# Optimization experiments

Hardware: AMD Instinct MI355X
Metric: run time of the kernel (lower is better)

The kernel has to match this reference:

```python
import jax, jax.numpy as jnp
import numpy as np

N, E = 50000, 800000
DIM, H, D = 256, 16, 8          # dim, num_heads, qk_dim
DH = D * H                      # 128
IN_RPE = 18
SCALE = D ** -0.5               # default qk_scale (None -> 1/sqrt(qk_dim))
EPS = 1e-16                     # torch_geometric softmax denominator eps


def setup_inputs() -> dict:
    key = jax.random.key(0)
    ks = jax.random.split(key, 10)
    x = jax.random.normal(ks[0], (N, DIM), dtype=jnp.float32)
    edge_index = jax.random.randint(ks[1], (2, E), 0, N, dtype=jnp.int64)
    edge_attr = jax.random.normal(ks[2], (E, IN_RPE), dtype=jnp.float32)
    # qkv Linear(dim -> 2*D*H + dim)
    Wqkv = jax.random.normal(ks[3], (DIM, 2 * DH + DIM), dtype=jnp.float32) * DIM ** -0.5
    bqkv = jnp.zeros((2 * DH + DIM,), dtype=jnp.float32)
    # k_rpe / q_rpe Linear(in_rpe_dim -> D*H) (heads_share_rpe=False)
    Wk_rpe = jax.random.normal(ks[4], (IN_RPE, DH), dtype=jnp.float32) * IN_RPE ** -0.5
    bk_rpe = jnp.zeros((DH,), dtype=jnp.float32)
    Wq_rpe = jax.random.normal(ks[5], (IN_RPE, DH), dtype=jnp.float32) * IN_RPE ** -0.5
    bq_rpe = jnp.zeros((DH,), dtype=jnp.float32)
    return {"x": x, "edge_index": edge_index, "edge_attr": edge_attr,
            "Wqkv": Wqkv, "bqkv": bqkv,
            "Wk_rpe": Wk_rpe, "bk_rpe": bk_rpe,
            "Wq_rpe": Wq_rpe, "bq_rpe": bq_rpe}


def _segment_softmax(compat, s, num_nodes):
    # numerically-stable softmax over edges grouped by source node s; compat: (E,H)
    m = jax.ops.segment_max(compat, s, num_segments=num_nodes)   # (N,H)
    ex = jnp.exp(compat - m[s])
    den = jax.ops.segment_sum(ex, s, num_segments=num_nodes)     # (N,H)
    return ex / (den[s] + EPS)


def reference(x, edge_index, edge_attr, Wqkv, bqkv, Wk_rpe, bk_rpe, Wq_rpe, bq_rpe):
    n = x.shape[0]
    e = edge_index.shape[1]
    qkv = x @ Wqkv + bqkv                      # (N, 2*DH + DIM)
    q = qkv[:, :DH].reshape(n, H, D)
    k = qkv[:, DH:2 * DH].reshape(n, H, D)
    v = qkv[:, 2 * DH:].reshape(n, H, DIM // H)
    s, t = edge_index[0], edge_index[1]
    qe = q[s] * SCALE                          # (E,H,D)
    ke = k[t]
    ke = ke + (edge_attr @ Wk_rpe + bk_rpe).reshape(e, H, D)
    qe = qe + (edge_attr @ Wq_rpe + bq_rpe).reshape(e, H, D)
    compat = jnp.einsum('ehd,ehd->eh', qe, ke)  # (E,H)
    attn = _segment_softmax(compat, s, n)       # (E,H)
    msg = (v[t] * attn[..., None]).reshape(e, DIM)  # (E,DIM)
    out = jax.ops.segment_sum(msg, s, num_segments=n)  # (N,DIM)
    return out
```

## Files before the change

### kernel.cpp

```cpp
#include <hip/hip_runtime.h>
#include <math.h>

#define DIMX   256
#define HEADS  16
#define QKD    8
#define DH     128
#define QKVW   512
#define INRPE  18
#define SCALE  0.35355339059327373f

typedef __attribute__((ext_vector_type(8))) short bf16x8;
typedef __attribute__((ext_vector_type(4))) float f32x4;

__device__ __forceinline__ void split1(float v, unsigned short& h, unsigned short& l)
{
    unsigned b  = __float_as_uint(v);
    unsigned hb = (b + 0x7FFFu + ((b >> 16) & 1u)) & 0xFFFF0000u;
    h = (unsigned short)(hb >> 16);
    float r = v - __uint_as_float(hb);
    unsigned rb = __float_as_uint(r);
    l = (unsigned short)((rb + 0x7FFFu + ((rb >> 16) & 1u)) >> 16);
}

__global__ __launch_bounds__(256) void convert_x(
    const float* __restrict__ x, unsigned short* __restrict__ xh,
    unsigned short* __restrict__ xl, int Nn, int Mpad)
{
    size_t total = (size_t)Mpad * 64;
    for (size_t i = (size_t)blockIdx.x * blockDim.x + threadIdx.x; i < total;
         i += (size_t)gridDim.x * blockDim.x) {
        size_t row = i >> 6;
        float4 v = make_float4(0.f, 0.f, 0.f, 0.f);
        if (row < (size_t)Nn) v = *(const float4*)&x[i * 4];
        ushort4 h, l;
        split1(v.x, h.x, l.x);
        split1(v.y, h.y, l.y);
        split1(v.z, h.z, l.z);
        split1(v.w, h.w, l.w);
        *(ushort4*)&xh[i * 4] = h;
        *(ushort4*)&xl[i * 4] = l;
    }
}

__global__ __launch_bounds__(256) void convert_w(
    const float* __restrict__ W, unsigned short* __restrict__ wth,
    unsigned short* __restrict__ wtl)
{
    int n = blockIdx.x;
    int k = threadIdx.x;
    float v = W[(size_t)k * QKVW + n];
    unsigned short h, l;
    split1(v, h, l);
    wth[(size_t)n * DIMX + k] = h;
    wtl[(size_t)n * DIMX + k] = l;
}

__global__ __launch_bounds__(256, 2) void qkv_gemm_mfma(
    const unsigned short* __restrict__ xh, const unsigned short* __restrict__ xl,
    const unsigned short* __restrict__ wth, const unsigned short* __restrict__ wtl,
    const float* __restrict__ bias, float* __restrict__ qkv, int Nn)
{
    int tid  = threadIdx.x;
    int w    = tid >> 6, lane = tid & 63;
    int wm   = w >> 1,   wn   = w & 1;
    int row0 = blockIdx.x * 128 + wm * 64;
    int col0 = blockIdx.y * 128 + wn * 64;
    int lrow = lane & 15;
    int lk8  = (lane >> 4) * 8;

    const unsigned short* pah = xh  + (size_t)(row0 + lrow) * DIMX + lk8;
    const unsigned short* pal = xl  + (size_t)(row0 + lrow) * DIMX + lk8;
    const unsigned short* pbh = wth + (size_t)(col0 + lrow) * DIMX + lk8;
    const unsigned short* pbl = wtl + (size_t)(col0 + lrow) * DIMX + lk8;

    f32x4 acc[4][4];
    #pragma unroll
    for (int i = 0; i < 4; i++)
        #pragma unroll
        for (int j = 0; j < 4; j++)
            acc[i][j] = (f32x4){0.f, 0.f, 0.f, 0.f};

    for (int t = 0; t < DIMX / 32; ++t) {
        int kb = t * 32;
        bf16x8 ah[4], al[4], bh[4], bl[4];
        #pragma unroll
        for (int f = 0; f < 4; ++f) {
            ah[f] = *(const bf16x8*)(pah + (size_t)f * 4096 + kb);
            al[f] = *(const bf16x8*)(pal + (size_t)f * 4096 + kb);
            bh[f] = *(const bf16x8*)(pbh + (size_t)f * 4096 + kb);
            bl[f] = *(const bf16x8*)(pbl + (size_t)f * 4096 + kb);
        }
        #pragma unroll
        for (int fm = 0; fm < 4; ++fm)
            #pragma unroll
            for (int fn = 0; fn < 4; ++fn) {
                acc[fm][fn] = __builtin_amdgcn_mfma_f32_16x16x32_bf16(
                    ah[fm], bh[fn], acc[fm][fn], 0, 0, 0);
                acc[fm][fn] = __builtin_amdgcn_mfma_f32_16x16x32_bf16(
                    ah[fm], bl[fn], acc[fm][fn], 0, 0, 0);
                acc[fm][fn] = __builtin_amdgcn_mfma_f32_16x16x32_bf16(
                    al[fm], bh[fn], acc[fm][fn], 0, 0, 0);
            }
    }

    float sc = (blockIdx.y == 0) ? SCALE : 1.0f;
    int rbase = (lane >> 4) * 4;
    #pragma unroll
    for (int fn = 0; fn < 4; ++fn) {
        float bv = bias[col0 + fn * 16 + lrow];
        #pragma unroll
        for (int fm = 0; fm < 4; ++fm) {
            #pragma unroll
            for (int j = 0; j < 4; ++j) {
                int r = row0 + fm * 16 + rbase + j;
                if (r < Nn)
                    qkv[(size_t)r * QKVW + col0 + fn * 16 + lrow] =
                        (acc[fm][fn][j] + bv) * sc;
            }
        }
    }
}

__global__ __launch_bounds__(256) void qkv_gemm(
    const float* __restrict__ x, const float* __restrict__ W,
    const float* __restrict__ bias, float* __restrict__ qkv, int Nn)
{
    __shared__ float As[16][132];
    __shared__ float Bs[16][132];

    int tid  = threadIdx.x;
    int row0 = blockIdx.x * 128;
    int col0 = blockIdx.y * 128;
    int tx = tid & 15, ty = tid >> 4;

    float acc[8][8] = {};

    for (int k0 = 0; k0 < DIMX; k0 += 16) {
        #pragma unroll
        for (int r = 0; r < 2; r++) {
            int idx  = tid + r * 256;
            int arow = idx >> 2, acol = (idx & 3) * 4;
            float4 av = make_float4(0.f, 0.f, 0.f, 0.f);
            int grow = row0 + arow;
            if (grow < Nn) av = *(const float4*)&x[(size_t)grow * DIMX + k0 + acol];
            As[acol + 0][arow] = av.x;
            As[acol + 1][arow] = av.y;
            As[acol + 2][arow] = av.z;
            As[acol + 3][arow] = av.w;
        }
        #pragma unroll
        for (int r = 0; r < 2; r++) {
            int idx  = tid + r * 256;
            int brow = idx >> 5, bcol = (idx & 31) * 4;
            float4 bv = *(const float4*)&W[(size_t)(k0 + brow) * QKVW + col0 + bcol];
            *(float4*)&Bs[brow][bcol] = bv;
        }
        __syncthreads();
        #pragma unroll
        for (int kk = 0; kk < 16; kk++) {
            float a0[8], b0[8];
            *(float4*)&a0[0] = *(const float4*)&As[kk][ty * 8];
            *(float4*)&a0[4] = *(const float4*)&As[kk][ty * 8 + 4];
            *(float4*)&b0[0] = *(const float4*)&Bs[kk][tx * 4];
            *(float4*)&b0[4] = *(const float4*)&Bs[kk][64 + tx * 4];
            #pragma unroll
            for (int i = 0; i < 8; i++)
                #pragma unroll
                for (int j = 0; j < 8; j++)
                    acc[i][j] = fmaf(a0[i], b0[j], acc[i][j]);
        }
        __syncthreads();
    }

    float4 bv0 = *(const float4*)&bias[col0 + tx * 4];
    float4 bv1 = *(const float4*)&bias[col0 + 64 + tx * 4];
    float sc = (col0 == 0) ? SCALE : 1.0f;
    #pragma unroll
    for (int i = 0; i < 8; i++) {
        int grow = row0 + ty * 8 + i;
        if (grow < Nn) {
            float4 o0, o1;
            o0.x = (acc[i][0] + bv0.x) * sc;
            o0.y = (acc[i][1] + bv0.y) * sc;
            o0.z = (acc[i][2] + bv0.z) * sc;
            o0.w = (acc[i][3] + bv0.w) * sc;
            o1.x = (acc[i][4] + bv1.x) * sc;
            o1.y = (acc[i][5] + bv1.y) * sc;
            o1.z = (acc[i][6] + bv1.z) * sc;
            o1.w = (acc[i][7] + bv1.w) * sc;
            *(float4*)&qkv[(size_t)grow * QKVW + col0 + tx * 4] = o0;
            *(float4*)&qkv[(size_t)grow * QKVW + col0 + 64 + tx * 4] = o1;
        }
    }
}

__global__ void count_kernel(const int* __restrict__ ei, int* __restrict__ deg, int E)
{
    int e = blockIdx.x * blockDim.x + threadIdx.x;
    if (e < E) atomicAdd(&deg[ei[e]], 1);
}

__device__ __forceinline__ int4 load_deg4(const int* __restrict__ deg, int base, int n)
{
    int4 v = make_int4(0, 0, 0, 0);
    if (base + 3 < n) v = *(const int4*)&deg[base];
    else {
        if (base + 0 < n) v.x = deg[base + 0];
        if (base + 1 < n) v.y = deg[base + 1];
        if (base + 2 < n) v.z = deg[base + 2];
        if (base + 3 < n) v.w = deg[base + 3];
    }
    return v;
}

__global__ __launch_bounds__(256) void scan_sums(
    const int* __restrict__ deg, int* __restrict__ psum, int n)
{
    int base = blockIdx.x * 1024 + threadIdx.x * 4;
    int4 v = load_deg4(deg, base, n);
    int s = v.x + v.y + v.z + v.w;
    #pragma unroll
    for (int d = 1; d < 64; d <<= 1) s += __shfl_xor(s, d, 64);
    __shared__ int ws[4];
    int lane = threadIdx.x & 63, w = threadIdx.x >> 6;
    if (lane == 0) ws[w] = s;
    __syncthreads();
    if (threadIdx.x == 0) psum[blockIdx.x] = ws[0] + ws[1] + ws[2] + ws[3];
}

__global__ __launch_bounds__(64) void scan_base(
    const int* __restrict__ psum, int* __restrict__ pbase,
    int* __restrict__ off, int n, int nchunk)
{
    int t = threadIdx.x;
    int carry = 0;
    for (int base = 0; base < nchunk; base += 64) {
        int v = (base + t < nchunk) ? psum[base + t] : 0;
        int incl = v;
        #pragma unroll
        for (int d = 1; d < 64; d <<= 1) {
            int u = __shfl_up(incl, d, 64);
            if (t >= d) incl += u;
        }
        if (base + t < nchunk) pbase[base + t] = carry + incl - v;
        carry += __shfl(incl, 63, 64);
    }
    if (t == 0) off[n] = carry;
}

__global__ __launch_bounds__(256) void scan_final(
    const int* __restrict__ deg, const int* __restrict__ pbase,
    int* __restrict__ off, int n)
{
    int base = blockIdx.x * 1024 + threadIdx.x * 4;
    int4 v = load_deg4(deg, base, n);
    int e1 = v.x, e2 = e1 + v.y, e3 = e2 + v.z, T = e3 + v.w;
    int lane = threadIdx.x & 63, w = threadIdx.x >> 6;
    int incl = T;
    #pragma unroll
    for (int d = 1; d < 64; d <<= 1) {
        int u = __shfl_up(incl, d, 64);
        if (lane >= d) incl += u;
    }
    int lexcl = incl - T;
    __shared__ int ws[4];
    if (lane == 63) ws[w] = incl;
    __syncthreads();
    int wexcl = 0;
    #pragma unroll
    for (int j = 0; j < 4; j++) if (j < w) wexcl += ws[j];
    int o0 = pbase[blockIdx.x] + wexcl + lexcl;
    if (base + 0 < n) off[base + 0] = o0;
    if (base + 1 < n) off[base + 1] = o0 + e1;
    if (base + 2 < n) off[base + 2] = o0 + e2;
    if (base + 3 < n) off[base + 3] = o0 + e3;
}

__global__ void scatter_kernel(const int* __restrict__ ei,
                               const int* __restrict__ off, int* __restrict__ cur,
                               int2* __restrict__ elist, int E)
{
    int e = blockIdx.x * blockDim.x + threadIdx.x;
    if (e < E) {
        int s = ei[e];
        int t = ei[E + e];
        int pos = atomicAdd(&cur[s], 1);
        elist[off[s] + pos] = make_int2(e, t);
    }
}

__global__ __launch_bounds__(128, 2) void node_attn(
    const float* __restrict__ qkv, const int2* __restrict__ elist,
    const int* __restrict__ off, const float* __restrict__ edge_attr,
    const float* __restrict__ Wq_rpe, const float* __restrict__ bq_rpe,
    const float* __restrict__ Wk_rpe, const float* __restrict__ bk_rpe,
    float* __restrict__ out, int Nn)
{
    int tid = threadIdx.x;

    float wq[INRPE], wk[INRPE];
    #pragma unroll
    for (int j = 0; j < INRPE; j++) {
        wq[j] = Wq_rpe[j * DH + tid];
        wk[j] = Wk_rpe[j * DH + tid];
    }
    #pragma unroll
    for (int j = 0; j < INRPE; j++) {
        asm volatile("" : "+v"(wq[j]), "+v"(wk[j]));
    }
    float bqv = bq_rpe[tid];
    float bkv = bk_rpe[tid];

    for (int n = blockIdx.x; n < Nn; n += gridDim.x) {
        int beg = off[n], end = off[n + 1];
        if (beg == end) {
            *(float2*)&out[(size_t)n * DIMX + 2 * tid] = make_float2(0.f, 0.f);
            continue;
        }
        float qs = qkv[(size_t)n * QKVW + tid] + bqv;

        float lsum = 0.0f;
        float2 o = make_float2(0.f, 0.f);

        int2 etA = elist[beg];
        int eA = __builtin_amdgcn_readfirstlane(etA.x);
        float  ktA = qkv[(size_t)etA.y * QKVW + DH + tid];
        float2 vtA = *(const float2*)&qkv[(size_t)etA.y * QKVW + 2 * DH + 2 * tid];
        float eaA[INRPE];
        {
            const float2* p = (const float2*)(edge_attr + (size_t)eA * INRPE);
            #pragma unroll
            for (int j = 0; j < 9; j++) { float2 u = p[j]; eaA[2*j] = u.x; eaA[2*j+1] = u.y; }
        }

        for (int i = beg; i < end; i += 2) {
            bool hasB = (i + 1 < end);
            float ktB = 0.f; float2 vtB = make_float2(0.f, 0.f);
            float eaB[INRPE];
            if (hasB) {
                int2 etB = elist[i + 1];
                int eB = __builtin_amdgcn_readfirstlane(etB.x);
                ktB = qkv[(size_t)etB.y * QKVW + DH + tid];
                vtB = *(const float2*)&qkv[(size_t)etB.y * QKVW + 2 * DH + 2 * tid];
                const float2* p = (const float2*)(edge_attr + (size_t)eB * INRPE);
                #pragma unroll
                for (int j = 0; j < 9; j++) { float2 u = p[j]; eaB[2*j] = u.x; eaB[2*j+1] = u.y; }
            }

            {
                float qr = 0.f, kr = bkv;
                #pragma unroll
                for (int j = 0; j < INRPE; j++) {
                    qr = fmaf(eaA[j], wq[j], qr);
                    kr = fmaf(eaA[j], wk[j], kr);
                }
                float c2 = (qs + qr) * (ktA + kr);
                c2 += __shfl_xor(c2, 1, 64);
                c2 += __shfl_xor(c2, 2, 64);
                c2 += __shfl_xor(c2, 4, 64);
                float ex = __expf(c2);
                lsum += ex;
                o.x = fmaf(ex, vtA.x, o.x);
                o.y = fmaf(ex, vtA.y, o.y);
            }

            if (i + 2 < end) {
                int2 et2 = elist[i + 2];
                int eN = __builtin_amdgcn_readfirstlane(et2.x);
                ktA = qkv[(size_t)et2.y * QKVW + DH + tid];
                vtA = *(const float2*)&qkv[(size_t)et2.y * QKVW + 2 * DH + 2 * tid];
                const float2* p = (const float2*)(edge_attr + (size_t)eN * INRPE);
                #pragma unroll
                for (int j = 0; j < 9; j++) { float2 u = p[j]; eaA[2*j] = u.x; eaA[2*j+1] = u.y; }
            }

            if (hasB) {
                float qr = 0.f, kr = bkv;
                #pragma unroll
                for (int j = 0; j < INRPE; j++) {
                    qr = fmaf(eaB[j], wq[j], qr);
                    kr = fmaf(eaB[j], wk[j], kr);
                }
                float c2 = (qs + qr) * (ktB + kr);
                c2 += __shfl_xor(c2, 1, 64);
                c2 += __shfl_xor(c2, 2, 64);
                c2 += __shfl_xor(c2, 4, 64);
                float ex = __expf(c2);
                lsum += ex;
                o.x = fmaf(ex, vtB.x, o.x);
                o.y = fmaf(ex, vtB.y, o.y);
            }
        }

        float inv = 1.0f / (lsum + 1e-16f);
        *(float2*)&out[(size_t)n * DIMX + 2 * tid] = make_float2(o.x * inv, o.y * inv);
    }
}

extern "C" void kernel_launch(void* const* d_in, const int* in_sizes, int n_in,
                              void* d_out, int out_size, void* d_ws, size_t ws_size,
                              hipStream_t stream)
{
    const float* x    = (const float*)d_in[0];
    const int*   ei   = (const int*)d_in[1];
    const float* ea   = (const float*)d_in[2];
    const float* Wqkv = (const float*)d_in[3];
    const float* bqkv = (const float*)d_in[4];
    const float* Wk   = (const float*)d_in[5];
    const float* bk   = (const float*)d_in[6];
    const float* Wq   = (const float*)d_in[7];
    const float* bq   = (const float*)d_in[8];

    int Nn = in_sizes[0] / DIMX;
    int E  = in_sizes[1] / 2;
    float* out = (float*)d_out;

    int Mblocks = (Nn + 127) / 128;
    int Mpad    = Mblocks * 128;
    int nchunk  = (Nn + 1023) / 1024;

    size_t qkv_bytes  = (size_t)Nn * QKVW * sizeof(float);
    float* qkv = (float*)d_ws;
    char*  P   = (char*)d_ws + qkv_bytes;

    size_t xpart  = (size_t)Mpad * DIMX * sizeof(unsigned short);
    size_t wpart  = (size_t)QKVW * DIMX * sizeof(unsigned short);
    size_t gemm_bytes = 2 * xpart + 2 * wpart;
    size_t csr_bytes  = sizeof(int) * (size_t)(3 * Nn + 2 + 2 * nchunk + 8)
                      + sizeof(int2) * (size_t)E;
    size_t need = qkv_bytes + (gemm_bytes > csr_bytes ? gemm_bytes : csr_bytes);

    int*  deg = (int*)P;
    int*  cur = deg + Nn;
    int*  off = cur + Nn;
    int2* elist = (int2*)(off + ((Nn + 2) & ~1));
    int*  psum  = (int*)(elist + E);
    int*  pbase = psum + nchunk;

    if (ws_size >= need) {
        unsigned short* xh  = (unsigned short*)P;
        unsigned short* xl  = xh + (size_t)Mpad * DIMX;
        unsigned short* wth = xl + (size_t)Mpad * DIMX;
        unsigned short* wtl = wth + (size_t)QKVW * DIMX;

        convert_x<<<2048, 256, 0, stream>>>(x, xh, xl, Nn, Mpad);
        convert_w<<<QKVW, 256, 0, stream>>>(Wqkv, wth, wtl);
        qkv_gemm_mfma<<<dim3(Mblocks, 4), 256, 0, stream>>>(xh, xl, wth, wtl,
                                                            bqkv, qkv, Nn);
    } else {
        qkv_gemm<<<dim3(Mblocks, QKVW / 128), 256, 0, stream>>>(x, Wqkv, bqkv, qkv, Nn);
    }

    hipMemsetAsync(deg, 0, sizeof(int) * 2 * (size_t)Nn, stream);
    count_kernel<<<(E + 255) / 256, 256, 0, stream>>>(ei, deg, E);
    scan_sums<<<nchunk, 256, 0, stream>>>(deg, psum, Nn);
    scan_base<<<1, 64, 0, stream>>>(psum, pbase, off, Nn, nchunk);
    scan_final<<<nchunk, 256, 0, stream>>>(deg, pbase, off, Nn);
    scatter_kernel<<<(E + 255) / 256, 256, 0, stream>>>(ei, off, cur, elist, E);

    int nb = 4096 < Nn ? 4096 : Nn;
    node_attn<<<nb, 128, 0, stream>>>(qkv, elist, off, ea, Wq, bq, Wk, bk, out, Nn);
}
```

Before: 656.3 us.

## Store V in bf16, split QK/V buffers, one block per node with prefetch

Measured after the change: 569.4 us. 13.2% less time.

```diff
diff --git a/kernel.cpp b/kernel.cpp
--- a/kernel.cpp
+++ b/kernel.cpp
@@ -20,6 +20,17 @@
     float r = v - __uint_as_float(hb);
     unsigned rb = __float_as_uint(r);
     l = (unsigned short)((rb + 0x7FFFu + ((rb >> 16) & 1u)) >> 16);
+}
+
+__device__ __forceinline__ unsigned short f2bf(float v)
+{
+    unsigned b = __float_as_uint(v);
+    return (unsigned short)((b + 0x7FFFu + ((b >> 16) & 1u)) >> 16);
+}
+
+__device__ __forceinline__ float bf2f(unsigned short u)
+{
+    return __uint_as_float((unsigned)u << 16);
 }
 
 __global__ __launch_bounds__(256) void convert_x(
@@ -58,7 +69,8 @@
 __global__ __launch_bounds__(256, 2) void qkv_gemm_mfma(
     const unsigned short* __restrict__ xh, const unsigned short* __restrict__ xl,
     const unsigned short* __restrict__ wth, const unsigned short* __restrict__ wtl,
-    const float* __restrict__ bias, float* __restrict__ qkv, int Nn)
+    const float* __restrict__ bias, float* __restrict__ qk,
+    unsigned short* __restrict__ vb, int Nn)
 {
     int tid  = threadIdx.x;
     int w    = tid >> 6, lane = tid & 63;
@@ -103,27 +115,44 @@
             }
     }
 
-    float sc = (blockIdx.y == 0) ? SCALE : 1.0f;
     int rbase = (lane >> 4) * 4;
-    #pragma unroll
-    for (int fn = 0; fn < 4; ++fn) {
-        float bv = bias[col0 + fn * 16 + lrow];
-        #pragma unroll
-        for (int fm = 0; fm < 4; ++fm) {
+    if (blockIdx.y < 2) {
+        float sc = (blockIdx.y == 0) ? SCALE : 1.0f;
+        #pragma unroll
+        for (int fn = 0; fn < 4; ++fn) {
+            float bv = bias[col0 + fn * 16 + lrow];
             #pragma unroll
-            for (int j = 0; j < 4; ++j) {
-                int r = row0 + fm * 16 + rbase + j;
-                if (r < Nn)
-                    qkv[(size_t)r * QKVW + col0 + fn * 16 + lrow] =
-                        (acc[fm][fn][j] + bv) * sc;
-            }
+            for (int fm = 0; fm < 4; ++fm)
+                #pragma unroll
+                for (int j = 0; j < 4; ++j) {
+                    int r = row0 + fm * 16 + rbase + j;
+                    if (r < Nn)
+                        qk[(size_t)r * 256 + col0 + fn * 16 + lrow] =
+                            (acc[fm][fn][j] + bv) * sc;
+                }
+        }
+    } else {
+        int vcol0 = col0 - 256;
+        #pragma unroll
+        for (int fn = 0; fn < 4; ++fn) {
+            float bv = bias[col0 + fn * 16 + lrow];
+            #pragma unroll
+            for (int fm = 0; fm < 4; ++fm)
+                #pragma unroll
+                for (int j = 0; j < 4; ++j) {
+                    int r = row0 + fm * 16 + rbase + j;
+                    if (r < Nn)
+                        vb[(size_t)r * 256 + vcol0 + fn * 16 + lrow] =
+                            f2bf(acc[fm][fn][j] + bv);
+                }
         }
     }
 }
 
 __global__ __launch_bounds__(256) void qkv_gemm(
     const float* __restrict__ x, const float* __restrict__ W,
-    const float* __restrict__ bias, float* __restrict__ qkv, int Nn)
+    const float* __restrict__ bias, float* __restrict__ qk,
+    unsigned short* __restrict__ vb, int Nn)
 {
     __shared__ float As[16][132];
     __shared__ float Bs[16][132];
@@ -174,22 +203,31 @@
 
     float4 bv0 = *(const float4*)&bias[col0 + tx * 4];
     float4 bv1 = *(const float4*)&bias[col0 + 64 + tx * 4];
+    bool isv = (col0 >= 256);
     float sc = (col0 == 0) ? SCALE : 1.0f;
     #pragma unroll
     for (int i = 0; i < 8; i++) {
         int grow = row0 + ty * 8 + i;
         if (grow < Nn) {
-            float4 o0, o1;
-            o0.x = (acc[i][0] + bv0.x) * sc;
-            o0.y = (acc[i][1] + bv0.y) * sc;
-            o0.z = (acc[i][2] + bv0.z) * sc;
-            o0.w = (acc[i][3] + bv0.w) * sc;
-            o1.x = (acc[i][4] + bv1.x) * sc;
-            o1.y = (acc[i][5] + bv1.y) * sc;
-            o1.z = (acc[i][6] + bv1.z) * sc;
-            o1.w = (acc[i][7] + bv1.w) * sc;
-            *(float4*)&qkv[(size_t)grow * QKVW + col0 + tx * 4] = o0;
-            *(float4*)&qkv[(size_t)grow * QKVW + col0 + 64 + tx * 4] = o1;
+            float o0[4], o1[4];
+            o0[0] = (acc[i][0] + bv0.x) * sc;
+            o0[1] = (acc[i][1] + bv0.y) * sc;
+            o0[2] = (acc[i][2] + bv0.z) * sc;
+            o0[3] = (acc[i][3] + bv0.w) * sc;
+            o1[0] = (acc[i][4] + bv1.x) * sc;
+            o1[1] = (acc[i][5] + bv1.y) * sc;
+            o1[2] = (acc[i][6] + bv1.z) * sc;
+            o1[3] = (acc[i][7] + bv1.w) * sc;
+            if (!isv) {
+                *(float4*)&qk[(size_t)grow * 256 + col0 + tx * 4] = *(float4*)o0;
+                *(float4*)&qk[(size_t)grow * 256 + col0 + 64 + tx * 4] = *(float4*)o1;
+            } else {
+                int vc = col0 - 256;
+                ushort4 u0 = make_ushort4(f2bf(o0[0]), f2bf(o0[1]), f2bf(o0[2]), f2bf(o0[3]));
+                ushort4 u1 = make_ushort4(f2bf(o1[0]), f2bf(o1[1]), f2bf(o1[2]), f2bf(o1[3]));
+                *(ushort4*)&vb[(size_t)grow * 256 + vc + tx * 4] = u0;
+                *(ushort4*)&vb[(size_t)grow * 256 + vc + 64 + tx * 4] = u1;
+            }
         }
     }
 }
@@ -290,13 +328,16 @@
 }
 
 __global__ __launch_bounds__(128, 2) void node_attn(
-    const float* __restrict__ qkv, const int2* __restrict__ elist,
-    const int* __restrict__ off, const float* __restrict__ edge_attr,
+    const float* __restrict__ qk, const unsigned short* __restrict__ vb,
+    const int2* __restrict__ elist, const int* __restrict__ off,
+    const float* __restrict__ edge_attr,
     const float* __restrict__ Wq_rpe, const float* __restrict__ bq_rpe,
     const float* __restrict__ Wk_rpe, const float* __restrict__ bk_rpe,
     float* __restrict__ out, int Nn)
 {
     int tid = threadIdx.x;
+    int n = blockIdx.x;
+    if (n >= Nn) return;
 
     float wq[INRPE], wk[INRPE];
     #pragma unroll
@@ -308,93 +349,69 @@
     for (int j = 0; j < INRPE; j++) {
         asm volatile("" : "+v"(wq[j]), "+v"(wk[j]));
     }
-    float bqv = bq_rpe[tid];
-    float bkv = bk_rpe[tid];
-
-    for (int n = blockIdx.x; n < Nn; n += gridDim.x) {
-        int beg = off[n], end = off[n + 1];
-        if (beg == end) {
-            *(float2*)&out[(size_t)n * DIMX + 2 * tid] = make_float2(0.f, 0.f);
-            continue;
-        }
-        float qs = qkv[(size_t)n * QKVW + tid] + bqv;
-
-        float lsum = 0.0f;
-        float2 o = make_float2(0.f, 0.f);
-
-        int2 etA = elist[beg];
-        int eA = __builtin_amdgcn_readfirstlane(etA.x);
-        float  ktA = qkv[(size_t)etA.y * QKVW + DH + tid];
-        float2 vtA = *(const float2*)&qkv[(size_t)etA.y * QKVW + 2 * DH + 2 * tid];
-        float eaA[INRPE];
+
+    float qs = qk[(size_t)n * 256 + tid] + bq_rpe[tid];
+    float bk = bk_rpe[tid];
+
+    int beg = off[n], end = off[n + 1];
+
+    if (beg == end) {
+        *(float2*)&out[(size_t)n * DIMX + 2 * tid] = make_float2(0.f, 0.f);
+        return;
+    }
+
+    float lsum = 0.0f;
+    float2 o = make_float2(0.f, 0.f);
+
+    int2 etc = elist[beg];
+    float   ktc = qk[(size_t)etc.y * 256 + DH + tid];
+    ushort2 vtc = *(const ushort2*)&vb[(size_t)etc.y * 256 + 2 * tid];
+    float eac[INRPE];
+    {
+        const float2* p = (const float2*)(edge_attr + (size_t)etc.x * INRPE);
+        #pragma unroll
+        for (int j = 0; j < 9; j++) { float2 v2 = p[j]; eac[2*j] = v2.x; eac[2*j+1] = v2.y; }
+    }
+    int2 etn = elist[(beg + 1 < end) ? beg + 1 : beg];
+
+    #pragma unroll 1
+    for (int i = beg; i < end; i++) {
+        int inx2 = (i + 2 < end) ? i + 2 : end - 1;
+        int2 et2 = elist[inx2];
+        float   ktn = qk[(size_t)etn.y * 256 + DH + tid];
+        ushort2 vtn = *(const ushort2*)&vb[(size_t)etn.y * 256 + 2 * tid];
+        float ean[INRPE];
         {
-            const float2* p = (const float2*)(edge_attr + (size_t)eA * INRPE);
+            const float2* p = (const float2*)(edge_attr + (size_t)etn.x * INRPE);
             #pragma unroll
-            for (int j = 0; j < 9; j++) { float2 u = p[j]; eaA[2*j] = u.x; eaA[2*j+1] = u.y; }
-        }
-
-        for (int i = beg; i < end; i += 2) {
-            bool hasB = (i + 1 < end);
-            float ktB = 0.f; float2 vtB = make_float2(0.f, 0.f);
-            float eaB[INRPE];
-            if (hasB) {
-                int2 etB = elist[i + 1];
-                int eB = __builtin_amdgcn_readfirstlane(etB.x);
-                ktB = qkv[(size_t)etB.y * QKVW + DH + tid];
-                vtB = *(const float2*)&qkv[(size_t)etB.y * QKVW + 2 * DH + 2 * tid];
-                const float2* p = (const float2*)(edge_attr + (size_t)eB * INRPE);
-                #pragma unroll
-                for (int j = 0; j < 9; j++) { float2 u = p[j]; eaB[2*j] = u.x; eaB[2*j+1] = u.y; }
-            }
-
-            {
-                float qr = 0.f, kr = bkv;
-                #pragma unroll
-                for (int j = 0; j < INRPE; j++) {
-                    qr = fmaf(eaA[j], wq[j], qr);
-                    kr = fmaf(eaA[j], wk[j], kr);
-                }
-                float c2 = (qs + qr) * (ktA + kr);
-                c2 += __shfl_xor(c2, 1, 64);
-                c2 += __shfl_xor(c2, 2, 64);
-                c2 += __shfl_xor(c2, 4, 64);
-                float ex = __expf(c2);
-                lsum += ex;
-                o.x = fmaf(ex, vtA.x, o.x);
-                o.y = fmaf(ex, vtA.y, o.y);
-            }
-
-            if (i + 2 < end) {
-                int2 et2 = elist[i + 2];
-                int eN = __builtin_amdgcn_readfirstlane(et2.x);
-                ktA = qkv[(size_t)et2.y * QKVW + DH + tid];
-                vtA = *(const float2*)&qkv[(size_t)et2.y * QKVW + 2 * DH + 2 * tid];
-                const float2* p = (const float2*)(edge_attr + (size_t)eN * INRPE);
-                #pragma unroll
-                for (int j = 0; j < 9; j++) { float2 u = p[j]; eaA[2*j] = u.x; eaA[2*j+1] = u.y; }
-            }
-
-            if (hasB) {
-                float qr = 0.f, kr = bkv;
-                #pragma unroll
-                for (int j = 0; j < INRPE; j++) {
-                    qr = fmaf(eaB[j], wq[j], qr);
-                    kr = fmaf(eaB[j], wk[j], kr);
-                }
-                float c2 = (qs + qr) * (ktB + kr);
-                c2 += __shfl_xor(c2, 1, 64);
-                c2 += __shfl_xor(c2, 2, 64);
-                c2 += __shfl_xor(c2, 4, 64);
-                float ex = __expf(c2);
-                lsum += ex;
-                o.x = fmaf(ex, vtB.x, o.x);
-                o.y = fmaf(ex, vtB.y, o.y);
-            }
-        }
-
-        float inv = 1.0f / (lsum + 1e-16f);
-        *(float2*)&out[(size_t)n * DIMX + 2 * tid] = make_float2(o.x * inv, o.y * inv);
-    }
+            for (int j = 0; j < 9; j++) { float2 v2 = p[j]; ean[2*j] = v2.x; ean[2*j+1] = v2.y; }
+        }
+
+        float qr = 0.f, kr = bk;
+        #pragma unroll
+        for (int j = 0; j < INRPE; j++) {
+            qr = fmaf(eac[j], wq[j], qr);
+            kr = fmaf(eac[j], wk[j], kr);
+        }
+
+        float c2 = (qs + qr) * (ktc + kr);
+        c2 += __shfl_xor(c2, 1, 64);
+        c2 += __shfl_xor(c2, 2, 64);
+        c2 += __shfl_xor(c2, 4, 64);
+
+        float ex = __expf(c2);
+        lsum += ex;
+        o.x = fmaf(ex, bf2f(vtc.x), o.x);
+        o.y = fmaf(ex, bf2f(vtc.y), o.y);
+
+        etc = etn; etn = et2;
+        ktc = ktn; vtc = vtn;
+        #pragma unroll
+        for (int j = 0; j < INRPE; j++) eac[j] = ean[j];
+    }
+
+    float inv = 1.0f / (lsum + 1e-16f);
+    *(float2*)&out[(size_t)n * DIMX + 2 * tid] = make_float2(o.x * inv, o.y * inv);
 }
 
 extern "C" void kernel_launch(void* const* d_in, const int* in_sizes, int n_in,
@@ -419,16 +436,19 @@
     int Mpad    = Mblocks * 128;
     int nchunk  = (Nn + 1023) / 1024;
 
-    size_t qkv_bytes  = (size_t)Nn * QKVW * sizeof(float);
-    float* qkv = (float*)d_ws;
-    char*  P   = (char*)d_ws + qkv_bytes;
+    size_t qk_bytes = (size_t)Nn * 256 * sizeof(float);
+    size_t vb_bytes = (size_t)Nn * 256 * sizeof(unsigned short);
+    float*          qkbuf = (float*)d_ws;
+    unsigned short* vbbuf = (unsigned short*)((char*)d_ws + qk_bytes);
+    char*           P     = (char*)d_ws + qk_bytes + vb_bytes;
 
     size_t xpart  = (size_t)Mpad * DIMX * sizeof(unsigned short);
     size_t wpart  = (size_t)QKVW * DIMX * sizeof(unsigned short);
     size_t gemm_bytes = 2 * xpart + 2 * wpart;
     size_t csr_bytes  = sizeof(int) * (size_t)(3 * Nn + 2 + 2 * nchunk + 8)
                       + sizeof(int2) * (size_t)E;
-    size_t need = qkv_bytes + (gemm_bytes > csr_bytes ? gemm_bytes : csr_bytes);
+    size_t need = qk_bytes + vb_bytes
+                + (gemm_bytes > csr_bytes ? gemm_bytes : csr_bytes);
 
     int*  deg = (int*)P;
     int*  cur = deg + Nn;
@@ -446,9 +466,10 @@
         convert_x<<<2048, 256, 0, stream>>>(x, xh, xl, Nn, Mpad);
         convert_w<<<QKVW, 256, 0, stream>>>(Wqkv, wth, wtl);
         qkv_gemm_mfma<<<dim3(Mblocks, 4), 256, 0, stream>>>(xh, xl, wth, wtl,
-                                                            bqkv, qkv, Nn);
+                                                            bqkv, qkbuf, vbbuf, Nn);
     } else {
-        qkv_gemm<<<dim3(Mblocks, QKVW / 128), 256, 0, stream>>>(x, Wqkv, bqkv, qkv, Nn);
+        qkv_gemm<<<dim3(Mblocks, QKVW / 128), 256, 0, stream>>>(x, Wqkv, bqkv,
+                                                                qkbuf, vbbuf, Nn);
     }
 
     hipMemsetAsync(deg, 0, sizeof(int) * 2 * (size_t)Nn, stream);
@@ -458,6 +479,6 @@
     scan_final<<<nchunk, 256, 0, stream>>>(deg, pbase, off, Nn);
     scatter_kernel<<<(E + 255) / 256, 256, 0, stream>>>(ei, off, cur, elist, E);
 
-    int nb = 4096 < Nn ? 4096 : Nn;
-    node_attn<<<nb, 128, 0, stream>>>(qkv, elist, off, ea, Wq, bq, Wk, bk, out, Nn);
-}
+    node_attn<<<Nn, 128, 0, stream>>>(qkbuf, vbbuf, elist, off, ea,
+                                      Wq, bq, Wk, bk, out, Nn);
+}
```

## Store K/V in fp16 split buffer and launch one block per node

Applied to the files above, without the earlier changes.

Measured after the change: 787.9 us. 20.1% more time.

```diff
diff --git a/kernel.cpp b/kernel.cpp
--- a/kernel.cpp
+++ b/kernel.cpp
@@ -1,4 +1,5 @@
 #include <hip/hip_runtime.h>
+#include <hip/hip_fp16.h>
 #include <math.h>
 
 #define DIMX   256
@@ -6,6 +7,7 @@
 #define QKD    8
 #define DH     128
 #define QKVW   512
+#define KVW    384
 #define INRPE  18
 #define SCALE  0.35355339059327373f
 
@@ -55,10 +57,11 @@
     wtl[(size_t)n * DIMX + k] = l;
 }
 
-__global__ __launch_bounds__(256, 2) void qkv_gemm_mfma(
+__global__ __launch_bounds__(256, 3) void qkv_gemm_mfma(
     const unsigned short* __restrict__ xh, const unsigned short* __restrict__ xl,
     const unsigned short* __restrict__ wth, const unsigned short* __restrict__ wtl,
-    const float* __restrict__ bias, float* __restrict__ qkv, int Nn)
+    const float* __restrict__ bias, float* __restrict__ qbuf,
+    __half* __restrict__ kvb, int Nn)
 {
     int tid  = threadIdx.x;
     int w    = tid >> 6, lane = tid & 63;
@@ -103,27 +106,43 @@
             }
     }
 
-    float sc = (blockIdx.y == 0) ? SCALE : 1.0f;
     int rbase = (lane >> 4) * 4;
-    #pragma unroll
-    for (int fn = 0; fn < 4; ++fn) {
-        float bv = bias[col0 + fn * 16 + lrow];
-        #pragma unroll
-        for (int fm = 0; fm < 4; ++fm) {
-            #pragma unroll
-            for (int j = 0; j < 4; ++j) {
-                int r = row0 + fm * 16 + rbase + j;
-                if (r < Nn)
-                    qkv[(size_t)r * QKVW + col0 + fn * 16 + lrow] =
-                        (acc[fm][fn][j] + bv) * sc;
-            }
+    if (blockIdx.y == 0) {
+        #pragma unroll
+        for (int fn = 0; fn < 4; ++fn) {
+            float bv = bias[col0 + fn * 16 + lrow];
+            #pragma unroll
+            for (int fm = 0; fm < 4; ++fm)
+                #pragma unroll
+                for (int j = 0; j < 4; ++j) {
+                    int r = row0 + fm * 16 + rbase + j;
+                    if (r < Nn)
+                        qbuf[(size_t)r * DH + col0 + fn * 16 + lrow] =
+                            (acc[fm][fn][j] + bv) * SCALE;
+                }
+        }
+    } else {
+        int base = col0 - 128;
+        #pragma unroll
+        for (int fn = 0; fn < 4; ++fn) {
+            float bv = bias[col0 + fn * 16 + lrow];
+            #pragma unroll
+            for (int fm = 0; fm < 4; ++fm)
+                #pragma unroll
+                for (int j = 0; j < 4; ++j) {
+                    int r = row0 + fm * 16 + rbase + j;
+                    if (r < Nn)
+                        kvb[(size_t)r * KVW + base + fn * 16 + lrow] =
+                            __float2half(acc[fm][fn][j] + bv);
+                }
         }
     }
 }
 
 __global__ __launch_bounds__(256) void qkv_gemm(
     const float* __restrict__ x, const float* __restrict__ W,
-    const float* __restrict__ bias, float* __restrict__ qkv, int Nn)
+    const float* __restrict__ bias, float* __restrict__ qbuf,
+    __half* __restrict__ kvb, int Nn)
 {
     __shared__ float As[16][132];
     __shared__ float Bs[16][132];
@@ -174,22 +193,29 @@
 
     float4 bv0 = *(const float4*)&bias[col0 + tx * 4];
     float4 bv1 = *(const float4*)&bias[col0 + 64 + tx * 4];
-    float sc = (col0 == 0) ? SCALE : 1.0f;
     #pragma unroll
     for (int i = 0; i < 8; i++) {
         int grow = row0 + ty * 8 + i;
         if (grow < Nn) {
-            float4 o0, o1;
-            o0.x = (acc[i][0] + bv0.x) * sc;
-            o0.y = (acc[i][1] + bv0.y) * sc;
-            o0.z = (acc[i][2] + bv0.z) * sc;
-            o0.w = (acc[i][3] + bv0.w) * sc;
-            o1.x = (acc[i][4] + bv1.x) * sc;
-            o1.y = (acc[i][5] + bv1.y) * sc;
-            o1.z = (acc[i][6] + bv1.z) * sc;
-            o1.w = (acc[i][7] + bv1.w) * sc;
-            *(float4*)&qkv[(size_t)grow * QKVW + col0 + tx * 4] = o0;
-            *(float4*)&qkv[(size_t)grow * QKVW + col0 + 64 + tx * 4] = o1;
+            float o0[4], o1[4];
+            o0[0] = acc[i][0] + bv0.x; o0[1] = acc[i][1] + bv0.y;
+            o0[2] = acc[i][2] + bv0.z; o0[3] = acc[i][3] + bv0.w;
+            o1[0] = acc[i][4] + bv1.x; o1[1] = acc[i][5] + bv1.y;
+            o1[2] = acc[i][6] + bv1.z; o1[3] = acc[i][7] + bv1.w;
+            if (col0 == 0) {
+                #pragma unroll
+                for (int j = 0; j < 4; j++) {
+                    qbuf[(size_t)grow * DH + tx * 4 + j]      = o0[j] * SCALE;
+                    qbuf[(size_t)grow * DH + 64 + tx * 4 + j] = o1[j] * SCALE;
+                }
+            } else {
+                int base = col0 - 128;
+                #pragma unroll
+                for (int j = 0; j < 4; j++) {
+                    kvb[(size_t)grow * KVW + base + tx * 4 + j]      = __float2half(o0[j]);
+                    kvb[(size_t)grow * KVW + base + 64 + tx * 4 + j] = __float2half(o1[j]);
+                }
+            }
         }
     }
 }
@@ -290,13 +316,15 @@
 }
 
 __global__ __launch_bounds__(128, 2) void node_attn(
-    const float* __restrict__ qkv, const int2* __restrict__ elist,
-    const int* __restrict__ off, const float* __restrict__ edge_attr,
+    const float* __restrict__ qbuf, const __half* __restrict__ kv,
+    const int2* __restrict__ elist, const int* __restrict__ off,
+    const float* __restrict__ edge_attr,
     const float* __restrict__ Wq_rpe, const float* __restrict__ bq_rpe,
     const float* __restrict__ Wk_rpe, const float* __restrict__ bk_rpe,
     float* __restrict__ out, int Nn)
 {
     int tid = threadIdx.x;
+    int n = blockIdx.x;
 
     float wq[INRPE], wk[INRPE];
     #pragma unroll
@@ -308,93 +336,91 @@
     for (int j = 0; j < INRPE; j++) {
         asm volatile("" : "+v"(wq[j]), "+v"(wk[j]));
     }
-    float bqv = bq_rpe[tid];
+
+    float qs = qbuf[(size_t)n * DH + tid] + bq_rpe[tid];
     float bkv = bk_rpe[tid];
 
-    for (int n = blockIdx.x; n < Nn; n += gridDim.x) {
-        int beg = off[n], end = off[n + 1];
-        if (beg == end) {
-            *(float2*)&out[(size_t)n * DIMX + 2 * tid] = make_float2(0.f, 0.f);
-            continue;
-        }
-        float qs = qkv[(size_t)n * QKVW + tid] + bqv;
-
-        float lsum = 0.0f;
-        float2 o = make_float2(0.f, 0.f);
-
-        int2 etA = elist[beg];
-        int eA = __builtin_amdgcn_readfirstlane(etA.x);
-        float  ktA = qkv[(size_t)etA.y * QKVW + DH + tid];
-        float2 vtA = *(const float2*)&qkv[(size_t)etA.y * QKVW + 2 * DH + 2 * tid];
-        float eaA[INRPE];
+    int beg = off[n], end = off[n + 1];
+    if (beg == end) {
+        *(float2*)&out[(size_t)n * DIMX + 2 * tid] = make_float2(0.f, 0.f);
+        return;
+    }
+
+    float lsum = 0.0f;
+    float2 o = make_float2(0.f, 0.f);
+
+    int2 etA = elist[beg];
+    __half  kA = kv[(size_t)etA.y * KVW + tid];
+    __half2 vA = *(const __half2*)&kv[(size_t)etA.y * KVW + DH + 2 * tid];
+    float eaA[INRPE];
+    {
+        const float2* p = (const float2*)(edge_attr + (size_t)etA.x * INRPE);
+        #pragma unroll
+        for (int j = 0; j < 9; j++) { float2 u = p[j]; eaA[2*j] = u.x; eaA[2*j+1] = u.y; }
+    }
+
+    for (int i = beg; i < end; i += 2) {
+        bool hasB = (i + 1 < end);
+        __half kB = __float2half(0.f);
+        __half2 vB = __half2(__float2half(0.f), __float2half(0.f));
+        float eaB[INRPE];
+        if (hasB) {
+            int2 etB = elist[i + 1];
+            kB = kv[(size_t)etB.y * KVW + tid];
+            vB = *(const __half2*)&kv[(size_t)etB.y * KVW + DH + 2 * tid];
+            const float2* p = (const float2*)(edge_attr + (size_t)etB.x * INRPE);
+            #pragma unroll
+            for (int j = 0; j < 9; j++) { float2 u = p[j]; eaB[2*j] = u.x; eaB[2*j+1] = u.y; }
+        }
+
         {
-            const float2* p = (const float2*)(edge_attr + (size_t)eA * INRPE);
+            float qr = 0.f, kr = bkv;
+            #pragma unroll
+            for (int j = 0; j < INRPE; j++) {
+                qr = fmaf(eaA[j], wq[j], qr);
+                kr = fmaf(eaA[j], wk[j], kr);
+            }
+            float c2 = (qs + qr) * (__half2float(kA) + kr);
+            c2 += __shfl_xor(c2, 1, 64);
+            c2 += __shfl_xor(c2, 2, 64);
+            c2 += __shfl_xor(c2, 4, 64);
+            float ex = __expf(c2);
+            float2 vf = __half22float2(vA);
+            lsum += ex;
+            o.x = fmaf(ex, vf.x, o.x);
+            o.y = fmaf(ex, vf.y, o.y);
+        }
+
+        if (i + 2 < end) {
+            int2 et2 = elist[i + 2];
+            kA = kv[(size_t)et2.y * KVW + tid];
+            vA = *(const __half2*)&kv[(size_t)et2.y * KVW + DH + 2 * tid];
+            const float2* p = (const float2*)(edge_attr + (size_t)et2.x * INRPE);
             #pragma unroll
             for (int j = 0; j < 9; j++) { float2 u = p[j]; eaA[2*j] = u.x; eaA[2*j+1] = u.y; }
         }
 
-        for (int i = beg; i < end; i += 2) {
-            bool hasB = (i + 1 < end);
-            float ktB = 0.f; float2 vtB = make_float2(0.f, 0.f);
-            float eaB[INRPE];
-            if (hasB) {
-                int2 etB = elist[i + 1];
-                int eB = __builtin_amdgcn_readfirstlane(etB.x);
-                ktB = qkv[(size_t)etB.y * QKVW + DH + tid];
-                vtB = *(const float2*)&qkv[(size_t)etB.y * QKVW + 2 * DH + 2 * tid];
-                const float2* p = (const float2*)(edge_attr + (size_t)eB * INRPE);
-                #pragma unroll
-                for (int j = 0; j < 9; j++) { float2 u = p[j]; eaB[2*j] = u.x; eaB[2*j+1] = u.y; }
+        if (hasB) {
+            float qr = 0.f, kr = bkv;
+            #pragma unroll
+            for (int j = 0; j < INRPE; j++) {
+                qr = fmaf(eaB[j], wq[j], qr);
+                kr = fmaf(eaB[j], wk[j], kr);
             }
-
-            {
-                float qr = 0.f, kr = bkv;
-                #pragma unroll
-                for (int j = 0; j < INRPE; j++) {
-                    qr = fmaf(eaA[j], wq[j], qr);
-                    kr = fmaf(eaA[j], wk[j], kr);
-                }
-                float c2 = (qs + qr) * (ktA + kr);
-                c2 += __shfl_xor(c2, 1, 64);
-                c2 += __shfl_xor(c2, 2, 64);
-                c2 += __shfl_xor(c2, 4, 64);
-                float ex = __expf(c2);
-                lsum += ex;
-                o.x = fmaf(ex, vtA.x, o.x);
-                o.y = fmaf(ex, vtA.y, o.y);
-            }
-
-            if (i + 2 < end) {
-                int2 et2 = elist[i + 2];
-                int eN = __builtin_amdgcn_readfirstlane(et2.x);
-                ktA = qkv[(size_t)et2.y * QKVW + DH + tid];
-                vtA = *(const float2*)&qkv[(size_t)et2.y * QKVW + 2 * DH + 2 * tid];
-                const float2* p = (const float2*)(edge_attr + (size_t)eN * INRPE);
-                #pragma unroll
-                for (int j = 0; j < 9; j++) { float2 u = p[j]; eaA[2*j] = u.x; eaA[2*j+1] = u.y; }
-            }
-
-            if (hasB) {
-                float qr = 0.f, kr = bkv;
-                #pragma unroll
-                for (int j = 0; j < INRPE; j++) {
-                    qr = fmaf(eaB[j], wq[j], qr);
-                    kr = fmaf(eaB[j], wk[j], kr);
-                }
-                float c2 = (qs + qr) * (ktB + kr);
-                c2 += __shfl_xor(c2, 1, 64);
-                c2 += __shfl_xor(c2, 2, 64);
-                c2 += __shfl_xor(c2, 4, 64);
-                float ex = __expf(c2);
-                lsum += ex;
-                o.x = fmaf(ex, vtB.x, o.x);
-                o.y = fmaf(ex, vtB.y, o.y);
-            }
-        }
-
-        float inv = 1.0f / (lsum + 1e-16f);
-        *(float2*)&out[(size_t)n * DIMX + 2 * tid] = make_float2(o.x * inv, o.y * inv);
-    }
+            float c2 = (qs + qr) * (__half2float(kB) + kr);
+            c2 += __shfl_xor(c2, 1, 64);
+            c2 += __shfl_xor(c2, 2, 64);
+            c2 += __shfl_xor(c2, 4, 64);
+            float ex = __expf(c2);
+            float2 vf = __half22float2(vB);
+            lsum += ex;
+            o.x = fmaf(ex, vf.x, o.x);
+            o.y = fmaf(ex, vf.y, o.y);
+        }
+    }
+
+    float inv = 1.0f / (lsum + 1e-16f);
+    *(float2*)&out[(size_t)n * DIMX + 2 * tid] = make_float2(o.x * inv, o.y * inv);
 }
 
 extern "C" void kernel_launch(void* const* d_in, const int* in_sizes, int n_in,
@@ -419,16 +445,19 @@
     int Mpad    = Mblocks * 128;
     int nchunk  = (Nn + 1023) / 1024;
 
-    size_t qkv_bytes  = (size_t)Nn * QKVW * sizeof(float);
-    float* qkv = (float*)d_ws;
-    char*  P   = (char*)d_ws + qkv_bytes;
+    size_t qb_bytes = (size_t)Nn * DH * sizeof(float);
+    size_t kv_bytes = (size_t)Nn * KVW * sizeof(__half);
+    float*  qbuf = (float*)d_ws;
+    __half* kvb  = (__half*)((char*)d_ws + qb_bytes);
+    char*   P    = (char*)d_ws + qb_bytes + kv_bytes;
 
     size_t xpart  = (size_t)Mpad * DIMX * sizeof(unsigned short);
     size_t wpart  = (size_t)QKVW * DIMX * sizeof(unsigned short);
     size_t gemm_bytes = 2 * xpart + 2 * wpart;
     size_t csr_bytes  = sizeof(int) * (size_t)(3 * Nn + 2 + 2 * nchunk + 8)
                       + sizeof(int2) * (size_t)E;
-    size_t need = qkv_bytes + (gemm_bytes > csr_bytes ? gemm_bytes : csr_bytes);
+    size_t need = qb_bytes + kv_bytes
+                + (gemm_bytes > csr_bytes ? gemm_bytes : csr_bytes);
 
     int*  deg = (int*)P;
     int*  cur = deg + Nn;
@@ -446,9 +475,10 @@
         convert_x<<<2048, 256, 0, stream>>>(x, xh, xl, Nn, Mpad);
         convert_w<<<QKVW, 256, 0, stream>>>(Wqkv, wth, wtl);
         qkv_gemm_mfma<<<dim3(Mblocks, 4), 256, 0, stream>>>(xh, xl, wth, wtl,
-                                                            bqkv, qkv, Nn);
+                                                            bqkv, qbuf, kvb, Nn);
     } else {
-        qkv_gemm<<<dim3(Mblocks, QKVW / 128), 256, 0, stream>>>(x, Wqkv, bqkv, qkv, Nn);
+        qkv_gemm<<<dim3(Mblocks, QKVW / 128), 256, 0, stream>>>(x, Wqkv, bqkv,
+                                                                qbuf, kvb, Nn);
     }
 
     hipMemsetAsync(deg, 0, sizeof(int) * 2 * (size_t)Nn, stream);
@@ -458,6 +488,6 @@
     scan_final<<<nchunk, 256, 0, stream>>>(deg, pbase, off, Nn);
     scatter_kernel<<<(E + 255) / 256, 256, 0, stream>>>(ei, off, cur, elist, E);
 
-    int nb = 4096 < Nn ? 4096 : Nn;
-    node_attn<<<nb, 128, 0, stream>>>(qkv, elist, off, ea, Wq, bq, Wk, bk, out, Nn);
-}
+    node_attn<<<Nn, 128, 0, stream>>>(qbuf, kvb, elist, off, ea,
+                                      Wq, bq, Wk, bk, out, Nn);
+}
```
